# Kernel optimization log

Measured on AMD Instinct MI355X. Metric: run time of the kernel, lower is better.

## Reference

```python
import jax, jax.numpy as jnp
import numpy as np

N_NODES = 100000
N_REL = 6
E_PER_REL = 100000
HID = 256
EMB = 256
N_GRAPHS = 128
N_NODE_TYPES = 4
SUBTYPE_BUCKETS = 256


def setup_inputs() -> dict:
    key = jax.random.key(0)
    ks = jax.random.split(key, 20)
    s = 0.05
    return {
        "x_type": jax.random.randint(ks[0], (N_NODES,), 0, N_NODE_TYPES),
        "x_sub": jax.random.randint(ks[1], (N_NODES,), 0, SUBTYPE_BUCKETS),
        "edges": jax.random.randint(ks[2], (N_REL, 2, E_PER_REL), 0, N_NODES),
        "batch_ids": jnp.sort(jax.random.randint(ks[3], (N_NODES,), 0, N_GRAPHS)),
        "n_graphs": N_GRAPHS,
        "type_emb": jax.random.normal(ks[4], (N_NODE_TYPES, HID // 2), jnp.float32) * s,
        "sub_emb": jax.random.normal(ks[5], (SUBTYPE_BUCKETS, HID // 2), jnp.float32) * s,
        "W_rel0": jax.random.normal(ks[6], (N_REL, HID, HID), jnp.float32) * s,
        "W_self0": jax.random.normal(ks[7], (HID, HID), jnp.float32) * s,
        "b0": jnp.zeros((HID,), jnp.float32),
        "W_rel1": jax.random.normal(ks[8], (N_REL, HID, HID), jnp.float32) * s,
        "W_self1": jax.random.normal(ks[9], (HID, HID), jnp.float32) * s,
        "b1": jnp.zeros((HID,), jnp.float32),
        "pW1": jax.random.normal(ks[10], (HID, HID), jnp.float32) * s,
        "pb1": jnp.zeros((HID,), jnp.float32),
        "pW2": jax.random.normal(ks[11], (HID, EMB), jnp.float32) * s,
        "pb2": jnp.zeros((EMB,), jnp.float32),
    }


def _rgcn_layer(h, edges, W_rel, W_self, b, n):
    # edges: (R, 2, E); h: (N, H)
    src, tgt = edges[:, 0, :], edges[:, 1, :]  # (R, E)
    # per-relation gather -> matmul: (R, E, H) @ (R, H, D) -> (R, E, D)
    msg = jnp.einsum('reh,rhd->red', h[src], W_rel)
    tgt_flat = tgt.reshape(-1)
    out = jax.ops.segment_sum(msg.reshape(-1, msg.shape[-1]), tgt_flat, num_segments=n)
    total_deg = jax.ops.segment_sum(jnp.ones_like(tgt_flat, dtype=h.dtype), tgt_flat, num_segments=n)
    total_deg = jnp.clip(total_deg, 1.0)[:, None]
    out = out / total_deg + h @ W_self + b
    return jax.nn.relu(out)


def _mean_pool(h, batch_ids, n_graphs):
    summed = jax.ops.segment_sum(h, batch_ids, num_segments=n_graphs)
    count = jax.ops.segment_sum(jnp.ones((h.shape[0],), h.dtype), batch_ids, num_segments=n_graphs)
    return summed / jnp.clip(count, 1.0)[:, None]


def reference(x_type, x_sub, edges, batch_ids, n_graphs, type_emb, sub_emb,
              W_rel0, W_self0, b0, W_rel1, W_self1, b1, pW1, pb1, pW2, pb2):
    n = x_type.shape[0]
    h = jnp.concatenate([type_emb[x_type], sub_emb[x_sub]], axis=-1)  # (N, HID)
    h = _rgcn_layer(h, edges, W_rel0, W_self0, b0, n)
    h = _rgcn_layer(h, edges, W_rel1, W_self1, b1, n)
    pooled = _mean_pool(h, batch_ids, n_graphs)  # (G, HID)
    return jax.nn.relu(pooled @ pW1 + pb1) @ pW2 + pb2  # (G, EMB)
```

## Files before the change

kernel.cpp:

```cpp
#include <hip/hip_runtime.h>

#define NN    100000
#define NEDGE 100000
#define NRELS 6
#define HIDD  256
#define NGR   128
#define NKEY  (NRELS * NN)
#define NEDGT (NRELS * NEDGE)
#define WFRAG_ELEMS (4 * 7 * 16 * 2 * 64 * 8)

typedef __bf16 bf16;
typedef __bf16 bf16x4 __attribute__((ext_vector_type(4)));
typedef __bf16 bf16x8 __attribute__((ext_vector_type(8)));
typedef float  f32x4  __attribute__((ext_vector_type(4)));
typedef float  f32x16 __attribute__((ext_vector_type(16)));

__device__ __forceinline__ float readlane_f(float v, int sl) {
    return __int_as_float(__builtin_amdgcn_readlane(__float_as_int(v), sl));
}

__global__ __launch_bounds__(256)
void hist_kernel(const int* __restrict__ edges, int* __restrict__ hist)
{
    int i = blockIdx.x * 256 + threadIdx.x;
    if (i >= NEDGT) return;
    int r = i / NEDGE;
    int e = i - r * NEDGE;
    int t = edges[r * (2 * NEDGE) + NEDGE + e];
    atomicAdd(&hist[r * NN + t], 1);
}

__global__ __launch_bounds__(256)
void scan_l0(const int* __restrict__ in, int* __restrict__ out, int* __restrict__ bsum, int n)
{
    __shared__ int sdata[256];
    const int t = threadIdx.x;
    const int base = blockIdx.x * 2048 + t * 8;
    int v[8]; int s = 0;
#pragma unroll
    for (int i = 0; i < 8; ++i) {
        int idx = base + i;
        int x = (idx < n) ? in[idx] : 0;
        v[i] = s; s += x;
    }
    sdata[t] = s;
    __syncthreads();
    for (int off = 1; off < 256; off <<= 1) {
        int y = (t >= off) ? sdata[t - off] : 0;
        __syncthreads();
        sdata[t] += y;
        __syncthreads();
    }
    int excl = sdata[t] - s;
#pragma unroll
    for (int i = 0; i < 8; ++i) {
        int idx = base + i;
        if (idx < n) out[idx] = excl + v[i];
    }
    if (t == 0) bsum[blockIdx.x] = sdata[255];
}

__global__ __launch_bounds__(256)
void scan_l1(int* __restrict__ bsum, int n)
{
    __shared__ int sdata[256];
    const int t = threadIdx.x;
    const int base = t * 8;
    int v[8]; int s = 0;
#pragma unroll
    for (int i = 0; i < 8; ++i) {
        int idx = base + i;
        int x = (idx < n) ? bsum[idx] : 0;
        v[i] = s; s += x;
    }
    sdata[t] = s;
    __syncthreads();
    for (int off = 1; off < 256; off <<= 1) {
        int y = (t >= off) ? sdata[t - off] : 0;
        __syncthreads();
        sdata[t] += y;
        __syncthreads();
    }
    int excl = sdata[t] - s;
#pragma unroll
    for (int i = 0; i < 8; ++i) {
        int idx = base + i;
        if (idx < n) bsum[idx] = excl + v[i];
    }
}

__global__ __launch_bounds__(256)
void scan_l2(int* __restrict__ offs, int* __restrict__ cursor, const int* __restrict__ bsum,
             const int* __restrict__ hist, float* __restrict__ invdeg, int n)
{
    int idx = blockIdx.x * 256 + threadIdx.x;
    if (idx == 0) offs[NKEY] = NEDGT;
    if (idx < NN) {
        int d = 0;
#pragma unroll
        for (int r = 0; r < NRELS; ++r) d += hist[r * NN + idx];
        invdeg[idx] = 1.0f / fmaxf((float)d, 1.0f);
    }
    if (idx >= n) return;
    int v = offs[idx] + bsum[idx >> 11];
    offs[idx] = v;
    cursor[idx] = v;
}

__global__ __launch_bounds__(256)
void scatter_kernel(const int* __restrict__ edges, int* __restrict__ cursor,
                    int* __restrict__ sorted_src, int* __restrict__ sorted_tgt)
{
    int i = blockIdx.x * 256 + threadIdx.x;
    if (i >= NEDGT) return;
    int r = i / NEDGE;
    int e = i - r * NEDGE;
    int s = edges[r * (2 * NEDGE) + e];
    int t = edges[r * (2 * NEDGE) + NEDGE + e];
    int pos = atomicAdd(&cursor[r * NN + t], 1);
    sorted_src[pos] = s;
    sorted_tgt[pos] = t;
}

__global__ __launch_bounds__(256)
void build_wfrag(const float* __restrict__ Wr0, const float* __restrict__ Ws0,
                 const float* __restrict__ Wr1, const float* __restrict__ Ws1,
                 bf16* __restrict__ Wf0, bf16* __restrict__ Wf1)
{
    const int seg = blockIdx.x;
    const int step = blockIdx.y;
    const int layer = blockIdx.z;
    const int tid = threadIdx.x;
    const int w = tid >> 6;
    const int lane = tid & 63;
    const int l31 = lane & 31;
    const int lhi = lane >> 5;

    const float* Wr = layer ? Wr1 : Wr0;
    const float* Ws = layer ? Ws1 : Ws0;
    const float* src = (seg < 6) ? (Wr + ((size_t)seg << 16)) : Ws;
    bf16* Wf = layer ? Wf1 : Wf0;

    const int kb = step * 16 + lhi * 8;
#pragma unroll
    for (int ct = 0; ct < 2; ++ct) {
        const int n = w * 64 + ct * 32 + l31;
        bf16x8 o;
#pragma unroll
        for (int j = 0; j < 8; ++j)
            o[j] = (bf16)src[(size_t)(kb + j) * 256 + n];
        const size_t fb_idx = (size_t)(((w * 7 + seg) * 16 + step) * 2 + ct) * 64 + lane;
        *(bf16x8*)(Wf + fb_idx * 8) = o;
    }
}

template<bool L0>
__global__ __launch_bounds__(256, 3)
void rgcn_fused(const bf16* __restrict__ hin,
                const int* __restrict__ xt, const int* __restrict__ xs,
                const float* __restrict__ temb, const float* __restrict__ semb,
                const bf16* __restrict__ Wfrag, const float* __restrict__ bias,
                const float* __restrict__ invdeg, const int* __restrict__ offs,
                const int* __restrict__ ssrc, const int* __restrict__ stgt,
                bf16* __restrict__ hout)
{
    constexpr int DEPTH = L0 ? 8 : 16;
    const int m0 = blockIdx.x * 64;
    const int tid = threadIdx.x;
    const int lane = tid & 63;
    const int w = tid >> 6;
    const int l31 = lane & 31;
    const int lhi = lane >> 5;
    const int rbase = w * 16;

    __shared__ __align__(16) bf16 As[64 * HIDD];

    f32x16 acc[2][2] = {};

    int ivrow = m0 + rbase + (lane & 15);
    if (ivrow >= NN) ivrow = NN - 1;
    const float ivreg = invdeg[ivrow];

    for (int seg = 0; seg < 7; ++seg) {
        __syncthreads();

#pragma unroll
        for (int z = 0; z < 8; ++z) {
            const int row = rbase + lhi * 8 + z;
            const int unit = row * 32 + (l31 ^ (row & 7));
            *(bf16x8*)&As[unit * 8] = (bf16x8)(bf16)0.0f;
        }

        if (seg == 6) {
#pragma unroll
            for (int z = 0; z < 8; ++z) {
                const int row = rbase + lhi * 8 + z;
                const int gr = m0 + row;
                if (gr < NN) {
                    bf16x8 o;
                    if (L0) {
                        const int f0 = l31 * 8;
                        const float* src = (f0 < 128) ? (temb + xt[gr] * 128 + f0)
                                                      : (semb + xs[gr] * 128 + (f0 - 128));
                        f32x4 x0 = *(const f32x4*)src;
                        f32x4 x1 = *(const f32x4*)(src + 4);
                        o[0] = (bf16)x0[0]; o[1] = (bf16)x0[1];
                        o[2] = (bf16)x0[2]; o[3] = (bf16)x0[3];
                        o[4] = (bf16)x1[0]; o[5] = (bf16)x1[1];
                        o[6] = (bf16)x1[2]; o[7] = (bf16)x1[3];
                    } else {
                        o = *(const bf16x8*)(hin + ((size_t)gr << 8) + l31 * 8);
                    }
                    const int unit = row * 32 + (l31 ^ (row & 7));
                    *(bf16x8*)&As[unit * 8] = o;
                }
            }
        } else {
            const int gr0 = m0 + rbase;
            if (gr0 < NN) {
                const int rend = (gr0 + 16 < NN) ? (gr0 + 16) : NN;
                int st = offs[seg * NN + gr0];
                const int en = offs[seg * NN + rend];

                float a0 = 0.f, a1 = 0.f, a2 = 0.f, a3 = 0.f;
                int cur = -1;

                while (st < en) {
                    const int cnt = (en - st < 64) ? (en - st) : 64;
                    const int idx = st + ((lane < cnt) ? lane : (cnt - 1));
                    const int sv = ssrc[idx];
                    const int tv = stgt[idx];
                    int at = 0, bt = 0;
                    if (L0) { at = xt[sv]; bt = xs[sv]; }

                    for (int base = 0; base < cnt; base += DEPTH) {
                        f32x4  fb[L0 ? DEPTH : 1];
                        bf16x4 hb[L0 ? 1 : DEPTH];
#pragma unroll
                        for (int p = 0; p < DEPTH; ++p) {
                            int ip = base + p;
                            ip = (ip < cnt) ? ip : (cnt - 1);
                            if (L0) {
                                const int a = __builtin_amdgcn_readlane(at, ip);
                                const int b = __builtin_amdgcn_readlane(bt, ip);
                                const float* srcp = (lane < 32)
                                    ? temb + a * 128 + lane * 4
                                    : semb + b * 128 + (lane - 32) * 4;
                                fb[p] = *(const f32x4*)srcp;
                            } else {
                                const int s = __builtin_amdgcn_readlane(sv, ip);
                                hb[p] = *(const bf16x4*)(hin + ((size_t)s << 8) + lane * 4);
                            }
                        }
#pragma unroll
                        for (int p = 0; p < DEPTH; ++p) {
                            if (base + p < cnt) {
                                const int t = __builtin_amdgcn_readlane(tv, base + p)
                                              - (m0 + rbase);
                                if (t != cur) {
                                    if (cur >= 0) {
                                        const float inv = readlane_f(ivreg, cur);
                                        bf16x4 o;
                                        o.x = (bf16)(a0 * inv); o.y = (bf16)(a1 * inv);
                                        o.z = (bf16)(a2 * inv); o.w = (bf16)(a3 * inv);
                                        const int row = rbase + cur;
                                        const int unit = row * 32 + ((lane >> 1) ^ (row & 7));
                                        *(bf16x4*)&As[unit * 8 + (lane & 1) * 4] = o;
                                    }
                                    cur = t; a0 = a1 = a2 = a3 = 0.f;
                                }
                                if (L0) {
                                    a0 += fb[p][0]; a1 += fb[p][1];
                                    a2 += fb[p][2]; a3 += fb[p][3];
                                } else {
                                    a0 += (float)hb[p].x; a1 += (float)hb[p].y;
                                    a2 += (float)hb[p].z; a3 += (float)hb[p].w;
                                }
                            }
                        }
                    }
                    st += cnt;
                }
                if (cur >= 0) {
                    const float inv = readlane_f(ivreg, cur);
                    bf16x4 o;
                    o.x = (bf16)(a0 * inv); o.y = (bf16)(a1 * inv);
                    o.z = (bf16)(a2 * inv); o.w = (bf16)(a3 * inv);
                    const int row = rbase + cur;
                    const int unit = row * 32 + ((lane >> 1) ^ (row & 7));
                    *(bf16x4*)&As[unit * 8 + (lane & 1) * 4] = o;
                }
            }
        }

        __syncthreads();

        const bf16* const wseg = Wfrag + ((size_t)((w * 7 + seg) * 16) * 2 * 64) * 8;
#pragma unroll
        for (int step = 0; step < 16; ++step) {
            bf16x8 b0 = *(const bf16x8*)(wseg + ((size_t)(step * 2 + 0) * 64 + lane) * 8);
            bf16x8 b1 = *(const bf16x8*)(wseg + ((size_t)(step * 2 + 1) * 64 + lane) * 8);
            const int ku = step * 2 + lhi;
            bf16x8 a0 = *(const bf16x8*)&As[(l31 * 32 + (ku ^ (l31 & 7))) * 8];
            bf16x8 a1 = *(const bf16x8*)&As[((32 + l31) * 32 + (ku ^ (l31 & 7))) * 8];
            acc[0][0] = __builtin_amdgcn_mfma_f32_32x32x16_bf16(a0, b0, acc[0][0], 0, 0, 0);
            acc[0][1] = __builtin_amdgcn_mfma_f32_32x32x16_bf16(a0, b1, acc[0][1], 0, 0, 0);
            acc[1][0] = __builtin_amdgcn_mfma_f32_32x32x16_bf16(a1, b0, acc[1][0], 0, 0, 0);
            acc[1][1] = __builtin_amdgcn_mfma_f32_32x32x16_bf16(a1, b1, acc[1][1], 0, 0, 0);
        }
    }

    float bcol[2];
#pragma unroll
    for (int ct = 0; ct < 2; ++ct) bcol[ct] = bias[w * 64 + ct * 32 + l31];
#pragma unroll
    for (int rt = 0; rt < 2; ++rt) {
#pragma unroll
        for (int reg = 0; reg < 16; ++reg) {
            const int row = m0 + rt * 32 + (reg & 3) + 8 * (reg >> 2) + 4 * lhi;
            if (row < NN) {
#pragma unroll
                for (int ct = 0; ct < 2; ++ct) {
                    const int col = w * 64 + ct * 32 + l31;
                    float v = acc[rt][ct][reg] + bcol[ct];
                    hout[((size_t)row << 8) + col] = (bf16)fmaxf(v, 0.0f);
                }
            }
        }
    }
}

#define PCHUNK 128
__global__ __launch_bounds__(256)
void pool_kernel(const bf16* __restrict__ h, const int* __restrict__ batch_ids,
                 float* __restrict__ pooled, float* __restrict__ cnt)
{
    const int n0 = blockIdx.x * PCHUNK;
    const int f = threadIdx.x;
    __shared__ int bid_l[PCHUNK];
    for (int i = f; i < PCHUNK; i += 256) {
        int n = n0 + i;
        bid_l[i] = (n < NN) ? batch_ids[n] : -1;
    }
    __syncthreads();
    const int nEnd = (NN - n0 < PCHUNK) ? (NN - n0) : PCHUNK;
    float s = 0.0f;
    int g = bid_l[0];
    int run = 0;
    for (int i = 0; i < nEnd; ++i) {
        int bg = bid_l[i];
        if (bg != g) {
            atomicAdd(&pooled[g * HIDD + f], s);
            if (f == 0) atomicAdd(&cnt[g], (float)run);
            s = 0.0f; run = 0; g = bg;
        }
        s += (float)h[(size_t)(n0 + i) * HIDD + f];
        run++;
    }
    if (run > 0) {
        atomicAdd(&pooled[g * HIDD + f], s);
        if (f == 0) atomicAdd(&cnt[g], (float)run);
    }
}

__global__ __launch_bounds__(256)
void mlp_kernel(const float* __restrict__ pooled, const float* __restrict__ cnt,
                const float* __restrict__ pW1, const float* __restrict__ pb1,
                const float* __restrict__ pW2, const float* __restrict__ pb2,
                float* __restrict__ out)
{
    const int g = blockIdx.x;
    const int d = threadIdx.x;
    __shared__ float pn[HIDD];
    __shared__ float mid[HIDD];
    float c = fmaxf(cnt[g], 1.0f);
    pn[d] = pooled[g * HIDD + d] / c;
    __syncthreads();
    float s = pb1[d];
    for (int k = 0; k < HIDD; ++k) s = fmaf(pn[k], pW1[k * HIDD + d], s);
    mid[d] = fmaxf(s, 0.0f);
    __syncthreads();
    float s2 = pb2[d];
    for (int k = 0; k < HIDD; ++k) s2 = fmaf(mid[k], pW2[k * HIDD + d], s2);
    out[g * HIDD + d] = s2;
}

extern "C" void kernel_launch(void* const* d_in, const int* in_sizes, int n_in,
                              void* d_out, int out_size, void* d_ws, size_t ws_size,
                              hipStream_t stream)
{
    const int*   x_type    = (const int*)d_in[0];
    const int*   x_sub     = (const int*)d_in[1];
    const int*   edges     = (const int*)d_in[2];
    const int*   batch_ids = (const int*)d_in[3];
    const float* type_emb  = (const float*)d_in[5];
    const float* sub_emb   = (const float*)d_in[6];
    const float* W_rel0    = (const float*)d_in[7];
    const float* W_self0   = (const float*)d_in[8];
    const float* b0        = (const float*)d_in[9];
    const float* W_rel1    = (const float*)d_in[10];
    const float* W_self1   = (const float*)d_in[11];
    const float* b1        = (const float*)d_in[12];
    const float* pW1       = (const float*)d_in[13];
    const float* pb1       = (const float*)d_in[14];
    const float* pW2       = (const float*)d_in[15];
    const float* pb2       = (const float*)d_in[16];
    float* out = (float*)d_out;

    char* p = (char*)d_ws;
    auto carve = [&](size_t bytes) { char* q = p; p += (bytes + 255) & ~255ull; return q; };
    bf16*  h1     = (bf16*) carve((size_t)NN * HIDD * sizeof(bf16));
    bf16*  h2     = (bf16*) carve((size_t)NN * HIDD * sizeof(bf16));
    bf16*  Wf0    = (bf16*) carve((size_t)WFRAG_ELEMS * sizeof(bf16));
    bf16*  Wf1    = (bf16*) carve((size_t)WFRAG_ELEMS * sizeof(bf16));
    float* invdeg = (float*)carve((size_t)NN * sizeof(float));
    int*   hist   = (int*)  carve((size_t)NKEY * sizeof(int));
    int*   offs   = (int*)  carve((size_t)(NKEY + 1) * sizeof(int));
    int*   cursor = (int*)  carve((size_t)NKEY * sizeof(int));
    int*   bsum   = (int*)  carve(2048 * sizeof(int));
    int*   ssrc   = (int*)  carve((size_t)NEDGT * sizeof(int));
    int*   stgt   = (int*)  carve((size_t)NEDGT * sizeof(int));
    float* pooled = (float*)carve((size_t)NGR * HIDD * sizeof(float));
    float* cnt    = (float*)carve((size_t)NGR * sizeof(float));

    hipMemsetAsync(hist, 0, (size_t)NKEY * sizeof(int), stream);
    hipMemsetAsync(pooled, 0, (size_t)(NGR * HIDD + NGR) * sizeof(float), stream);

    const int NB0 = (NKEY + 2047) / 2048;
    hist_kernel<<<(NEDGT + 255) / 256, 256, 0, stream>>>(edges, hist);
    scan_l0<<<NB0, 256, 0, stream>>>(hist, offs, bsum, NKEY);
    scan_l1<<<1, 256, 0, stream>>>(bsum, NB0);
    scan_l2<<<(NKEY + 255) / 256, 256, 0, stream>>>(offs, cursor, bsum, hist, invdeg, NKEY);
    scatter_kernel<<<(NEDGT + 255) / 256, 256, 0, stream>>>(edges, cursor, ssrc, stgt);

    dim3 wgrid(7, 16, 2);
    build_wfrag<<<wgrid, 256, 0, stream>>>(W_rel0, W_self0, W_rel1, W_self1, Wf0, Wf1);

    const int FGRID = (NN + 63) / 64;
    rgcn_fused<true><<<FGRID, 256, 0, stream>>>(nullptr, x_type, x_sub, type_emb, sub_emb,
                                                Wf0, b0, invdeg, offs, ssrc, stgt, h1);
    rgcn_fused<false><<<FGRID, 256, 0, stream>>>(h1, x_type, x_sub, type_emb, sub_emb,
                                                 Wf1, b1, invdeg, offs, ssrc, stgt, h2);

    pool_kernel<<<(NN + PCHUNK - 1) / PCHUNK, 256, 0, stream>>>(h2, batch_ids, pooled, cnt);
    mlp_kernel<<<NGR, 256, 0, stream>>>(pooled, cnt, pW1, pb1, pW2, pb2, out);
}
```

Measured before the change: 593.5 us.

## Double-buffer LDS tile to overlap next-relation gather with MFMA; pack edge src/tgt

The fused RGCN layer kernel now uses two LDS A-tiles. It prefetches the first gather batch of the next relation segment into registers, runs the current segment's MFMAs, and then consumes the next segment. This overlaps the gather latency with the matrix work and removes one barrier per segment. The sorted edge arrays are packed into one int, holding the source index plus the low 4 bits of the target as a local row, which halves index traffic. In exchange, occupancy drops to 2 waves per SIMD, and LDS and register use rise.

Measured after the change: 762.5 us. +28.5%, slower.

```diff
diff --git a/kernel.cpp b/kernel.cpp
--- a/kernel.cpp
+++ b/kernel.cpp
@@ -8,6 +8,7 @@
 #define NKEY  (NRELS * NN)
 #define NEDGT (NRELS * NEDGE)
 #define WFRAG_ELEMS (4 * 7 * 16 * 2 * 64 * 8)
+#define SMASK 0xFFFFF
 
 typedef __bf16 bf16;
 typedef __bf16 bf16x4 __attribute__((ext_vector_type(4)));
@@ -109,7 +110,7 @@
 
 __global__ __launch_bounds__(256)
 void scatter_kernel(const int* __restrict__ edges, int* __restrict__ cursor,
-                    int* __restrict__ sorted_src, int* __restrict__ sorted_tgt)
+                    int* __restrict__ epack)
 {
     int i = blockIdx.x * 256 + threadIdx.x;
     if (i >= NEDGT) return;
@@ -118,8 +119,7 @@
     int s = edges[r * (2 * NEDGE) + e];
     int t = edges[r * (2 * NEDGE) + NEDGE + e];
     int pos = atomicAdd(&cursor[r * NN + t], 1);
-    sorted_src[pos] = s;
-    sorted_tgt[pos] = t;
+    epack[pos] = s | ((t & 15) << 24);
 }
 
 __global__ __launch_bounds__(256)
@@ -155,14 +155,13 @@
 }
 
 template<bool L0>
-__global__ __launch_bounds__(256, 3)
+__global__ __launch_bounds__(256, 2)
 void rgcn_fused(const bf16* __restrict__ hin,
                 const int* __restrict__ xt, const int* __restrict__ xs,
                 const float* __restrict__ temb, const float* __restrict__ semb,
                 const bf16* __restrict__ Wfrag, const float* __restrict__ bias,
                 const float* __restrict__ invdeg, const int* __restrict__ offs,
-                const int* __restrict__ ssrc, const int* __restrict__ stgt,
-                bf16* __restrict__ hout)
+                const int* __restrict__ epack, bf16* __restrict__ hout)
 {
     constexpr int DEPTH = L0 ? 8 : 16;
     const int m0 = blockIdx.x * 64;
@@ -172,128 +171,201 @@
     const int l31 = lane & 31;
     const int lhi = lane >> 5;
     const int rbase = w * 16;
-
-    __shared__ __align__(16) bf16 As[64 * HIDD];
+    const int gr0 = m0 + rbase;
+
+    __shared__ __align__(16) bf16 As[2][64 * HIDD];
 
     f32x16 acc[2][2] = {};
 
-    int ivrow = m0 + rbase + (lane & 15);
+    int ivrow = gr0 + (lane & 15);
     if (ivrow >= NN) ivrow = NN - 1;
     const float ivreg = invdeg[ivrow];
 
-    for (int seg = 0; seg < 7; ++seg) {
-        __syncthreads();
-
+    int st_all[6], en_all[6];
+#pragma unroll
+    for (int s = 0; s < 6; ++s) { st_all[s] = 0; en_all[s] = 0; }
+    if (gr0 < NN) {
+        const int rend = (gr0 + 16 < NN) ? (gr0 + 16) : NN;
+#pragma unroll
+        for (int s = 0; s < 6; ++s) {
+            st_all[s] = offs[s * NN + gr0];
+            en_all[s] = offs[s * NN + rend];
+        }
+    }
+
+    int pf_pv = 0, pf_at = 0, pf_bt = 0;
+    f32x4  pf_fb[L0 ? DEPTH : 1];
+    bf16x4 pf_hb[L0 ? 1 : DEPTH];
+    bf16x8 pf_self[8];
+
+    auto prefetch_seg = [&](int s) {
+        if (s == 6) {
+#pragma unroll
+            for (int z = 0; z < 8; ++z) {
+                int gr = gr0 + lhi * 8 + z;
+                if (gr >= NN) gr = NN - 1;
+                if constexpr (L0) {
+                    const int f0 = l31 * 8;
+                    const float* src = (f0 < 128) ? (temb + xt[gr] * 128 + f0)
+                                                  : (semb + xs[gr] * 128 + (f0 - 128));
+                    f32x4 x0 = *(const f32x4*)src;
+                    f32x4 x1 = *(const f32x4*)(src + 4);
+                    bf16x8 o;
+                    o[0] = (bf16)x0[0]; o[1] = (bf16)x0[1];
+                    o[2] = (bf16)x0[2]; o[3] = (bf16)x0[3];
+                    o[4] = (bf16)x1[0]; o[5] = (bf16)x1[1];
+                    o[6] = (bf16)x1[2]; o[7] = (bf16)x1[3];
+                    pf_self[z] = o;
+                } else {
+                    pf_self[z] = *(const bf16x8*)(hin + ((size_t)gr << 8) + l31 * 8);
+                }
+            }
+            return;
+        }
+        const int st = st_all[s], en = en_all[s];
+        if (st < en) {
+            const int cnt = (en - st < 64) ? (en - st) : 64;
+            const int idx = st + ((lane < cnt) ? lane : (cnt - 1));
+            pf_pv = epack[idx];
+            if constexpr (L0) {
+                const int sl = pf_pv & SMASK;
+                pf_at = xt[sl]; pf_bt = xs[sl];
+            }
+#pragma unroll
+            for (int p = 0; p < DEPTH; ++p) {
+                const int ip = (p < cnt) ? p : (cnt - 1);
+                if constexpr (L0) {
+                    const int a = __builtin_amdgcn_readlane(pf_at, ip);
+                    const int b = __builtin_amdgcn_readlane(pf_bt, ip);
+                    const float* srcp = (lane < 32)
+                        ? temb + a * 128 + lane * 4
+                        : semb + b * 128 + (lane - 32) * 4;
+                    pf_fb[p] = *(const f32x4*)srcp;
+                } else {
+                    const int sl = __builtin_amdgcn_readlane(pf_pv, ip) & SMASK;
+                    pf_hb[p] = *(const bf16x4*)(hin + ((size_t)sl << 8) + lane * 4);
+                }
+            }
+        }
+    };
+
+    auto zero_rows = [&](int buf) {
 #pragma unroll
         for (int z = 0; z < 8; ++z) {
             const int row = rbase + lhi * 8 + z;
             const int unit = row * 32 + (l31 ^ (row & 7));
-            *(bf16x8*)&As[unit * 8] = (bf16x8)(bf16)0.0f;
-        }
-
-        if (seg == 6) {
+            *(bf16x8*)&As[buf][unit * 8] = (bf16x8)(bf16)0.0f;
+        }
+    };
+
+    auto consume_seg = [&](int s, int buf) {
+        if (s == 6) {
 #pragma unroll
             for (int z = 0; z < 8; ++z) {
                 const int row = rbase + lhi * 8 + z;
-                const int gr = m0 + row;
-                if (gr < NN) {
-                    bf16x8 o;
-                    if (L0) {
-                        const int f0 = l31 * 8;
-                        const float* src = (f0 < 128) ? (temb + xt[gr] * 128 + f0)
-                                                      : (semb + xs[gr] * 128 + (f0 - 128));
-                        f32x4 x0 = *(const f32x4*)src;
-                        f32x4 x1 = *(const f32x4*)(src + 4);
-                        o[0] = (bf16)x0[0]; o[1] = (bf16)x0[1];
-                        o[2] = (bf16)x0[2]; o[3] = (bf16)x0[3];
-                        o[4] = (bf16)x1[0]; o[5] = (bf16)x1[1];
-                        o[6] = (bf16)x1[2]; o[7] = (bf16)x1[3];
-                    } else {
-                        o = *(const bf16x8*)(hin + ((size_t)gr << 8) + l31 * 8);
+                const int unit = row * 32 + (l31 ^ (row & 7));
+                *(bf16x8*)&As[buf][unit * 8] = pf_self[z];
+            }
+            return;
+        }
+        int st = st_all[s];
+        const int en = en_all[s];
+        if (st >= en) return;
+
+        float a0 = 0.f, a1 = 0.f, a2 = 0.f, a3 = 0.f;
+        int cur = -1;
+        int pv = pf_pv, at = pf_at, bt = pf_bt;
+        bool pf_valid = true;
+
+        while (st < en) {
+            const int cnt = (en - st < 64) ? (en - st) : 64;
+            if (!pf_valid) {
+                const int idx = st + ((lane < cnt) ? lane : (cnt - 1));
+                pv = epack[idx];
+                if constexpr (L0) {
+                    const int sl = pv & SMASK;
+                    at = xt[sl]; bt = xs[sl];
+                }
+            }
+            for (int base = 0; base < cnt; base += DEPTH) {
+                f32x4  fb[L0 ? DEPTH : 1];
+                bf16x4 hb[L0 ? 1 : DEPTH];
+                if (pf_valid && base == 0) {
+#pragma unroll
+                    for (int p = 0; p < DEPTH; ++p) {
+                        if constexpr (L0) fb[p] = pf_fb[p];
+                        else              hb[p] = pf_hb[p];
                     }
-                    const int unit = row * 32 + (l31 ^ (row & 7));
-                    *(bf16x8*)&As[unit * 8] = o;
-                }
-            }
-        } else {
-            const int gr0 = m0 + rbase;
-            if (gr0 < NN) {
-                const int rend = (gr0 + 16 < NN) ? (gr0 + 16) : NN;
-                int st = offs[seg * NN + gr0];
-                const int en = offs[seg * NN + rend];
-
-                float a0 = 0.f, a1 = 0.f, a2 = 0.f, a3 = 0.f;
-                int cur = -1;
-
-                while (st < en) {
-                    const int cnt = (en - st < 64) ? (en - st) : 64;
-                    const int idx = st + ((lane < cnt) ? lane : (cnt - 1));
-                    const int sv = ssrc[idx];
-                    const int tv = stgt[idx];
-                    int at = 0, bt = 0;
-                    if (L0) { at = xt[sv]; bt = xs[sv]; }
-
-                    for (int base = 0; base < cnt; base += DEPTH) {
-                        f32x4  fb[L0 ? DEPTH : 1];
-                        bf16x4 hb[L0 ? 1 : DEPTH];
-#pragma unroll
-                        for (int p = 0; p < DEPTH; ++p) {
-                            int ip = base + p;
-                            ip = (ip < cnt) ? ip : (cnt - 1);
-                            if (L0) {
-                                const int a = __builtin_amdgcn_readlane(at, ip);
-                                const int b = __builtin_amdgcn_readlane(bt, ip);
-                                const float* srcp = (lane < 32)
-                                    ? temb + a * 128 + lane * 4
-                                    : semb + b * 128 + (lane - 32) * 4;
-                                fb[p] = *(const f32x4*)srcp;
-                            } else {
-                                const int s = __builtin_amdgcn_readlane(sv, ip);
-                                hb[p] = *(const bf16x4*)(hin + ((size_t)s << 8) + lane * 4);
-                            }
-                        }
-#pragma unroll
-                        for (int p = 0; p < DEPTH; ++p) {
-                            if (base + p < cnt) {
-                                const int t = __builtin_amdgcn_readlane(tv, base + p)
-                                              - (m0 + rbase);
-                                if (t != cur) {
-                                    if (cur >= 0) {
-                                        const float inv = readlane_f(ivreg, cur);
-                                        bf16x4 o;
-                                        o.x = (bf16)(a0 * inv); o.y = (bf16)(a1 * inv);
-                                        o.z = (bf16)(a2 * inv); o.w = (bf16)(a3 * inv);
-                                        const int row = rbase + cur;
-                                        const int unit = row * 32 + ((lane >> 1) ^ (row & 7));
-                                        *(bf16x4*)&As[unit * 8 + (lane & 1) * 4] = o;
-                                    }
-                                    cur = t; a0 = a1 = a2 = a3 = 0.f;
-                                }
-                                if (L0) {
-                                    a0 += fb[p][0]; a1 += fb[p][1];
-                                    a2 += fb[p][2]; a3 += fb[p][3];
-                                } else {
-                                    a0 += (float)hb[p].x; a1 += (float)hb[p].y;
-                                    a2 += (float)hb[p].z; a3 += (float)hb[p].w;
-                                }
-                            }
+                } else {
+#pragma unroll
+                    for (int p = 0; p < DEPTH; ++p) {
+                        int ip = base + p;
+                        ip = (ip < cnt) ? ip : (cnt - 1);
+                        if constexpr (L0) {
+                            const int a = __builtin_amdgcn_readlane(at, ip);
+                            const int b = __builtin_amdgcn_readlane(bt, ip);
+                            const float* srcp = (lane < 32)
+                                ? temb + a * 128 + lane * 4
+                                : semb + b * 128 + (lane - 32) * 4;
+                            fb[p] = *(const f32x4*)srcp;
+                        } else {
+                            const int sl = __builtin_amdgcn_readlane(pv, ip) & SMASK;
+                            hb[p] = *(const bf16x4*)(hin + ((size_t)sl << 8) + lane * 4);
                         }
                     }
-                    st += cnt;
                 }
-                if (cur >= 0) {
-                    const float inv = readlane_f(ivreg, cur);
-                    bf16x4 o;
-                    o.x = (bf16)(a0 * inv); o.y = (bf16)(a1 * inv);
-                    o.z = (bf16)(a2 * inv); o.w = (bf16)(a3 * inv);
-                    const int row = rbase + cur;
-                    const int unit = row * 32 + ((lane >> 1) ^ (row & 7));
-                    *(bf16x4*)&As[unit * 8 + (lane & 1) * 4] = o;
+#pragma unroll
+                for (int p = 0; p < DEPTH; ++p) {
+                    if (base + p < cnt) {
+                        const int t = __builtin_amdgcn_readlane(pv, base + p) >> 24;
+                        if (t != cur) {
+                            if (cur >= 0) {
+                                const float inv = readlane_f(ivreg, cur);
+                                bf16x4 o;
+                                o.x = (bf16)(a0 * inv); o.y = (bf16)(a1 * inv);
+                                o.z = (bf16)(a2 * inv); o.w = (bf16)(a3 * inv);
+                                const int row = rbase + cur;
+                                const int unit = row * 32 + ((lane >> 1) ^ (row & 7));
+                                *(bf16x4*)&As[buf][unit * 8 + (lane & 1) * 4] = o;
+                            }
+                            cur = t; a0 = a1 = a2 = a3 = 0.f;
+                        }
+                        if constexpr (L0) {
+                            a0 += fb[p][0]; a1 += fb[p][1];
+                            a2 += fb[p][2]; a3 += fb[p][3];
+                        } else {
+                            a0 += (float)hb[p].x; a1 += (float)hb[p].y;
+                            a2 += (float)hb[p].z; a3 += (float)hb[p].w;
+                        }
+                    }
                 }
             }
-        }
-
-        __syncthreads();
+            st += cnt;
+            pf_valid = false;
+        }
+        if (cur >= 0) {
+            const float inv = readlane_f(ivreg, cur);
+            bf16x4 o;
+            o.x = (bf16)(a0 * inv); o.y = (bf16)(a1 * inv);
+            o.z = (bf16)(a2 * inv); o.w = (bf16)(a3 * inv);
+            const int row = rbase + cur;
+            const int unit = row * 32 + ((lane >> 1) ^ (row & 7));
+            *(bf16x4*)&As[buf][unit * 8 + (lane & 1) * 4] = o;
+        }
+    };
+
+    zero_rows(0);
+    prefetch_seg(0);
+    consume_seg(0, 0);
+    __syncthreads();
+
+    for (int seg = 0; seg < 7; ++seg) {
+        const int cur = seg & 1, nxt = cur ^ 1;
+
+        if (seg < 6) {
+            prefetch_seg(seg + 1);
+            if (seg + 1 != 6) zero_rows(nxt);
+        }
 
         const bf16* const wseg = Wfrag + ((size_t)((w * 7 + seg) * 16) * 2 * 64) * 8;
 #pragma unroll
@@ -301,13 +373,16 @@
             bf16x8 b0 = *(const bf16x8*)(wseg + ((size_t)(step * 2 + 0) * 64 + lane) * 8);
             bf16x8 b1 = *(const bf16x8*)(wseg + ((size_t)(step * 2 + 1) * 64 + lane) * 8);
             const int ku = step * 2 + lhi;
-            bf16x8 a0 = *(const bf16x8*)&As[(l31 * 32 + (ku ^ (l31 & 7))) * 8];
-            bf16x8 a1 = *(const bf16x8*)&As[((32 + l31) * 32 + (ku ^ (l31 & 7))) * 8];
+            bf16x8 a0 = *(const bf16x8*)&As[cur][(l31 * 32 + (ku ^ (l31 & 7))) * 8];
+            bf16x8 a1 = *(const bf16x8*)&As[cur][((32 + l31) * 32 + (ku ^ (l31 & 7))) * 8];
             acc[0][0] = __builtin_amdgcn_mfma_f32_32x32x16_bf16(a0, b0, acc[0][0], 0, 0, 0);
             acc[0][1] = __builtin_amdgcn_mfma_f32_32x32x16_bf16(a0, b1, acc[0][1], 0, 0, 0);
             acc[1][0] = __builtin_amdgcn_mfma_f32_32x32x16_bf16(a1, b0, acc[1][0], 0, 0, 0);
             acc[1][1] = __builtin_amdgcn_mfma_f32_32x32x16_bf16(a1, b1, acc[1][1], 0, 0, 0);
         }
+
+        if (seg < 6) consume_seg(seg + 1, nxt);
+        __syncthreads();
     }
 
     float bcol[2];
@@ -418,8 +493,7 @@
     int*   offs   = (int*)  carve((size_t)(NKEY + 1) * sizeof(int));
     int*   cursor = (int*)  carve((size_t)NKEY * sizeof(int));
     int*   bsum   = (int*)  carve(2048 * sizeof(int));
-    int*   ssrc   = (int*)  carve((size_t)NEDGT * sizeof(int));
-    int*   stgt   = (int*)  carve((size_t)NEDGT * sizeof(int));
+    int*   epack  = (int*)  carve((size_t)NEDGT * sizeof(int));
     float* pooled = (float*)carve((size_t)NGR * HIDD * sizeof(float));
     float* cnt    = (float*)carve((size_t)NGR * sizeof(float));
 
@@ -431,16 +505,16 @@
     scan_l0<<<NB0, 256, 0, stream>>>(hist, offs, bsum, NKEY);
     scan_l1<<<1, 256, 0, stream>>>(bsum, NB0);
     scan_l2<<<(NKEY + 255) / 256, 256, 0, stream>>>(offs, cursor, bsum, hist, invdeg, NKEY);
-    scatter_kernel<<<(NEDGT + 255) / 256, 256, 0, stream>>>(edges, cursor, ssrc, stgt);
+    scatter_kernel<<<(NEDGT + 255) / 256, 256, 0, stream>>>(edges, cursor, epack);
 
     dim3 wgrid(7, 16, 2);
     build_wfrag<<<wgrid, 256, 0, stream>>>(W_rel0, W_self0, W_rel1, W_self1, Wf0, Wf1);
 
     const int FGRID = (NN + 63) / 64;
     rgcn_fused<true><<<FGRID, 256, 0, stream>>>(nullptr, x_type, x_sub, type_emb, sub_emb,
-                                                Wf0, b0, invdeg, offs, ssrc, stgt, h1);
+                                                Wf0, b0, invdeg, offs, epack, h1);
     rgcn_fused<false><<<FGRID, 256, 0, stream>>>(h1, x_type, x_sub, type_emb, sub_emb,
-                                                 Wf1, b1, invdeg, offs, ssrc, stgt, h2);
+                                                 Wf1, b1, invdeg, offs, epack, h2);
 
     pool_kernel<<<(NN + PCHUNK - 1) / PCHUNK, 256, 0, stream>>>(h2, batch_ids, pooled, cnt);
     mlp_kernel<<<NGR, 256, 0, stream>>>(pooled, cnt, pW1, pb1, pW2, pb2, out);
```

## Fuse mean-pool into layer-2 epilogue and pack edge src/tgt into one int

Applied to the files above, without the earlier changes.

The second RGCN layer now reduces its ReLU output rows straight into per-graph pooled sums with atomics, so the h2 buffer write and the separate pool kernel are gone. Node counts per graph are computed in scan_l2 with a wave ballot. Sorted edges are stored as one packed int (20-bit source plus 4-bit local target row) instead of two arrays, which halves edge index traffic. The cost is an epilogue loop over the graphs present in each tile and more float atomics on pooled.

Measured after the change: 540.5 us. -8.9%, faster.

```diff
diff --git a/kernel.cpp b/kernel.cpp
--- a/kernel.cpp
+++ b/kernel.cpp
@@ -8,6 +8,7 @@
 #define NKEY  (NRELS * NN)
 #define NEDGT (NRELS * NEDGE)
 #define WFRAG_ELEMS (4 * 7 * 16 * 2 * 64 * 8)
+#define SMASK 0xFFFFF
 
 typedef __bf16 bf16;
 typedef __bf16 bf16x4 __attribute__((ext_vector_type(4)));
@@ -91,10 +92,27 @@
 
 __global__ __launch_bounds__(256)
 void scan_l2(int* __restrict__ offs, int* __restrict__ cursor, const int* __restrict__ bsum,
-             const int* __restrict__ hist, float* __restrict__ invdeg, int n)
+             const int* __restrict__ hist, float* __restrict__ invdeg,
+             const int* __restrict__ batch_ids, float* __restrict__ cnt, int n)
 {
     int idx = blockIdx.x * 256 + threadIdx.x;
     if (idx == 0) offs[NKEY] = NEDGT;
+
+    {
+        const int lane = threadIdx.x & 63;
+        const bool valid = idx < NN;
+        const int gv = valid ? batch_ids[idx] : -1;
+        const int gprev = __shfl(gv, lane - 1);
+        const bool head = valid && (lane == 0 || gv != gprev);
+        const bool stop = head || !valid;
+        const unsigned long long mask = __ballot(stop);
+        if (head) {
+            unsigned long long above = (lane == 63) ? 0ull : (mask >> (lane + 1));
+            const int next = above ? (lane + 1 + __builtin_ctzll(above)) : 64;
+            atomicAdd(&cnt[gv], (float)(next - lane));
+        }
+    }
+
     if (idx < NN) {
         int d = 0;
 #pragma unroll
@@ -109,7 +127,7 @@
 
 __global__ __launch_bounds__(256)
 void scatter_kernel(const int* __restrict__ edges, int* __restrict__ cursor,
-                    int* __restrict__ sorted_src, int* __restrict__ sorted_tgt)
+                    int* __restrict__ epack)
 {
     int i = blockIdx.x * 256 + threadIdx.x;
     if (i >= NEDGT) return;
@@ -118,8 +136,7 @@
     int s = edges[r * (2 * NEDGE) + e];
     int t = edges[r * (2 * NEDGE) + NEDGE + e];
     int pos = atomicAdd(&cursor[r * NN + t], 1);
-    sorted_src[pos] = s;
-    sorted_tgt[pos] = t;
+    epack[pos] = s | ((t & 15) << 20);
 }
 
 __global__ __launch_bounds__(256)
@@ -154,15 +171,15 @@
     }
 }
 
-template<bool L0>
+template<bool L0, bool POOL>
 __global__ __launch_bounds__(256, 3)
 void rgcn_fused(const bf16* __restrict__ hin,
                 const int* __restrict__ xt, const int* __restrict__ xs,
                 const float* __restrict__ temb, const float* __restrict__ semb,
                 const bf16* __restrict__ Wfrag, const float* __restrict__ bias,
                 const float* __restrict__ invdeg, const int* __restrict__ offs,
-                const int* __restrict__ ssrc, const int* __restrict__ stgt,
-                bf16* __restrict__ hout)
+                const int* __restrict__ epack, const int* __restrict__ batch_ids,
+                float* __restrict__ pooled, bf16* __restrict__ hout)
 {
     constexpr int DEPTH = L0 ? 8 : 16;
     const int m0 = blockIdx.x * 64;
@@ -228,10 +245,9 @@
                 while (st < en) {
                     const int cnt = (en - st < 64) ? (en - st) : 64;
                     const int idx = st + ((lane < cnt) ? lane : (cnt - 1));
-                    const int sv = ssrc[idx];
-                    const int tv = stgt[idx];
+                    const int pv = epack[idx];
                     int at = 0, bt = 0;
-                    if (L0) { at = xt[sv]; bt = xs[sv]; }
+                    if (L0) { const int sl = pv & SMASK; at = xt[sl]; bt = xs[sl]; }
 
                     for (int base = 0; base < cnt; base += DEPTH) {
                         f32x4  fb[L0 ? DEPTH : 1];
@@ -248,15 +264,14 @@
                                     : semb + b * 128 + (lane - 32) * 4;
                                 fb[p] = *(const f32x4*)srcp;
                             } else {
-                                const int s = __builtin_amdgcn_readlane(sv, ip);
+                                const int s = __builtin_amdgcn_readlane(pv, ip) & SMASK;
                                 hb[p] = *(const bf16x4*)(hin + ((size_t)s << 8) + lane * 4);
                             }
                         }
 #pragma unroll
                         for (int p = 0; p < DEPTH; ++p) {
                             if (base + p < cnt) {
-                                const int t = __builtin_amdgcn_readlane(tv, base + p)
-                                              - (m0 + rbase);
+                                const int t = __builtin_amdgcn_readlane(pv, base + p) >> 20;
                                 if (t != cur) {
                                     if (cur >= 0) {
                                         const float inv = readlane_f(ivreg, cur);
@@ -313,53 +328,54 @@
     float bcol[2];
 #pragma unroll
     for (int ct = 0; ct < 2; ++ct) bcol[ct] = bias[w * 64 + ct * 32 + l31];
-#pragma unroll
-    for (int rt = 0; rt < 2; ++rt) {
-#pragma unroll
-        for (int reg = 0; reg < 16; ++reg) {
-            const int row = m0 + rt * 32 + (reg & 3) + 8 * (reg >> 2) + 4 * lhi;
-            if (row < NN) {
-#pragma unroll
-                for (int ct = 0; ct < 2; ++ct) {
-                    const int col = w * 64 + ct * 32 + l31;
-                    float v = acc[rt][ct][reg] + bcol[ct];
-                    hout[((size_t)row << 8) + col] = (bf16)fmaxf(v, 0.0f);
+
+    if constexpr (POOL) {
+        __syncthreads();
+        int* bidArr = (int*)As;
+        if (tid < 64) {
+            const int r = m0 + tid;
+            bidArr[tid] = (r < NN) ? batch_ids[r] : -1;
+        }
+        __syncthreads();
+        const int last = (m0 + 63 < NN) ? 63 : (NN - 1 - m0);
+        const int glo = bidArr[0];
+        const int ghi = bidArr[last];
+        for (int g = glo; g <= ghi; ++g) {
+            float s0 = 0.f, s1 = 0.f;
+#pragma unroll
+            for (int rt = 0; rt < 2; ++rt) {
+#pragma unroll
+                for (int reg = 0; reg < 16; ++reg) {
+                    const int rl = rt * 32 + (reg & 3) + 8 * (reg >> 2) + 4 * lhi;
+                    if (bidArr[rl] == g) {
+                        s0 += fmaxf(acc[rt][0][reg] + bcol[0], 0.0f);
+                        s1 += fmaxf(acc[rt][1][reg] + bcol[1], 0.0f);
+                    }
                 }
             }
-        }
-    }
-}
-
-#define PCHUNK 128
-__global__ __launch_bounds__(256)
-void pool_kernel(const bf16* __restrict__ h, const int* __restrict__ batch_ids,
-                 float* __restrict__ pooled, float* __restrict__ cnt)
-{
-    const int n0 = blockIdx.x * PCHUNK;
-    const int f = threadIdx.x;
-    __shared__ int bid_l[PCHUNK];
-    for (int i = f; i < PCHUNK; i += 256) {
-        int n = n0 + i;
-        bid_l[i] = (n < NN) ? batch_ids[n] : -1;
-    }
-    __syncthreads();
-    const int nEnd = (NN - n0 < PCHUNK) ? (NN - n0) : PCHUNK;
-    float s = 0.0f;
-    int g = bid_l[0];
-    int run = 0;
-    for (int i = 0; i < nEnd; ++i) {
-        int bg = bid_l[i];
-        if (bg != g) {
-            atomicAdd(&pooled[g * HIDD + f], s);
-            if (f == 0) atomicAdd(&cnt[g], (float)run);
-            s = 0.0f; run = 0; g = bg;
-        }
-        s += (float)h[(size_t)(n0 + i) * HIDD + f];
-        run++;
-    }
-    if (run > 0) {
-        atomicAdd(&pooled[g * HIDD + f], s);
-        if (f == 0) atomicAdd(&cnt[g], (float)run);
+            s0 += __shfl_xor(s0, 32);
+            s1 += __shfl_xor(s1, 32);
+            if (lhi == 0) {
+                atomicAdd(&pooled[g * HIDD + w * 64 + l31], s0);
+                atomicAdd(&pooled[g * HIDD + w * 64 + 32 + l31], s1);
+            }
+        }
+    } else {
+#pragma unroll
+        for (int rt = 0; rt < 2; ++rt) {
+#pragma unroll
+            for (int reg = 0; reg < 16; ++reg) {
+                const int row = m0 + rt * 32 + (reg & 3) + 8 * (reg >> 2) + 4 * lhi;
+                if (row < NN) {
+#pragma unroll
+                    for (int ct = 0; ct < 2; ++ct) {
+                        const int col = w * 64 + ct * 32 + l31;
+                        float v = acc[rt][ct][reg] + bcol[ct];
+                        hout[((size_t)row << 8) + col] = (bf16)fmaxf(v, 0.0f);
+                    }
+                }
+            }
+        }
     }
 }
 
@@ -410,7 +426,6 @@
     char* p = (char*)d_ws;
     auto carve = [&](size_t bytes) { char* q = p; p += (bytes + 255) & ~255ull; return q; };
     bf16*  h1     = (bf16*) carve((size_t)NN * HIDD * sizeof(bf16));
-    bf16*  h2     = (bf16*) carve((size_t)NN * HIDD * sizeof(bf16));
     bf16*  Wf0    = (bf16*) carve((size_t)WFRAG_ELEMS * sizeof(bf16));
     bf16*  Wf1    = (bf16*) carve((size_t)WFRAG_ELEMS * sizeof(bf16));
     float* invdeg = (float*)carve((size_t)NN * sizeof(float));
@@ -418,8 +433,7 @@
     int*   offs   = (int*)  carve((size_t)(NKEY + 1) * sizeof(int));
     int*   cursor = (int*)  carve((size_t)NKEY * sizeof(int));
     int*   bsum   = (int*)  carve(2048 * sizeof(int));
-    int*   ssrc   = (int*)  carve((size_t)NEDGT * sizeof(int));
-    int*   stgt   = (int*)  carve((size_t)NEDGT * sizeof(int));
+    int*   epack  = (int*)  carve((size_t)NEDGT * sizeof(int));
     float* pooled = (float*)carve((size_t)NGR * HIDD * sizeof(float));
     float* cnt    = (float*)carve((size_t)NGR * sizeof(float));
 
@@ -430,18 +444,20 @@
     hist_kernel<<<(NEDGT + 255) / 256, 256, 0, stream>>>(edges, hist);
     scan_l0<<<NB0, 256, 0, stream>>>(hist, offs, bsum, NKEY);
     scan_l1<<<1, 256, 0, stream>>>(bsum, NB0);
-    scan_l2<<<(NKEY + 255) / 256, 256, 0, stream>>>(offs, cursor, bsum, hist, invdeg, NKEY);
-    scatter_kernel<<<(NEDGT + 255) / 256, 256, 0, stream>>>(edges, cursor, ssrc, stgt);
+    scan_l2<<<(NKEY + 255) / 256, 256, 0, stream>>>(offs, cursor, bsum, hist, invdeg,
+                                                    batch_ids, cnt, NKEY);
+    scatter_kernel<<<(NEDGT + 255) / 256, 256, 0, stream>>>(edges, cursor, epack);
 
     dim3 wgrid(7, 16, 2);
     build_wfrag<<<wgrid, 256, 0, stream>>>(W_rel0, W_self0, W_rel1, W_self1, Wf0, Wf1);
 
     const int FGRID = (NN + 63) / 64;
-    rgcn_fused<true><<<FGRID, 256, 0, stream>>>(nullptr, x_type, x_sub, type_emb, sub_emb,
-                                                Wf0, b0, invdeg, offs, ssrc, stgt, h1);
-    rgcn_fused<false><<<FGRID, 256, 0, stream>>>(h1, x_type, x_sub, type_emb, sub_emb,
-                                                 Wf1, b1, invdeg, offs, ssrc, stgt, h2);
-
-    pool_kernel<<<(NN + PCHUNK - 1) / PCHUNK, 256, 0, stream>>>(h2, batch_ids, pooled, cnt);
+    rgcn_fused<true, false><<<FGRID, 256, 0, stream>>>(
+        nullptr, x_type, x_sub, type_emb, sub_emb,
+        Wf0, b0, invdeg, offs, epack, batch_ids, pooled, h1);
+    rgcn_fused<false, true><<<FGRID, 256, 0, stream>>>(
+        h1, x_type, x_sub, type_emb, sub_emb,
+        Wf1, b1, invdeg, offs, epack, batch_ids, pooled, nullptr);
+
     mlp_kernel<<<NGR, 256, 0, stream>>>(pooled, cnt, pW1, pb1, pW2, pb2, out);
 }
```
